# Kernel optimization log

Measured on AMD Instinct MI355X. Metric: run time of the kernel, lower is better.

Reference implementation:

```python
import jax, jax.numpy as jnp
import numpy as np
import math

H = 16          # num_attention_heads
D = 64          # attention_head_size
MAX_POS = 1024  # max_position_embeddings


def setup_inputs() -> dict:
    key = jax.random.key(0)
    ks = jax.random.split(key, 6)
    B, S, HID = 4, 1024, 1024
    scale = 1.0 / math.sqrt(HID)
    return {
        "hidden_states": jax.random.normal(ks[0], (B, S, HID), jnp.float32),
        "attention_mask": jnp.zeros((B, 1, 1, S), jnp.float32),
        "Wq": jax.random.normal(ks[1], (HID, HID), jnp.float32) * scale,
        "bq": jnp.zeros((HID,), jnp.float32),
        "Wk": jax.random.normal(ks[2], (HID, HID), jnp.float32) * scale,
        "bk": jnp.zeros((HID,), jnp.float32),
        "Wv": jax.random.normal(ks[3], (HID, HID), jnp.float32) * scale,
        "bv": jnp.zeros((HID,), jnp.float32),
        "dist_emb": jax.random.normal(ks[4], (2 * MAX_POS - 1, D), jnp.float32) * 0.02,
    }


def _split_heads(x):
    # [B,S,H*D] -> [B,H,S,D]
    B, S, _ = x.shape
    return x.reshape(B, S, H, D).transpose(0, 2, 1, 3)


def reference(hidden_states, attention_mask, Wq, bq, Wk, bk, Wv, bv, dist_emb):
    B, S, _ = hidden_states.shape
    q = _split_heads(hidden_states @ Wq.T + bq)   # [B,H,S,D]
    k = _split_heads(hidden_states @ Wk.T + bk)
    v = _split_heads(hidden_states @ Wv.T + bv)

    scores = jnp.einsum("bhqd,bhkd->bhqk", q, k)  # [B,H,S,S]

    # relative_key_query positional bias
    pos_l = jnp.arange(S)[:, None]
    pos_r = jnp.arange(S)[None, :]
    distance = pos_l - pos_r + (MAX_POS - 1)      # [S,S] in [0, 2*MAX_POS-2]
    pos_emb = dist_emb[distance]                  # [S,S,D]
    rel_q = jnp.einsum("bhld,lrd->bhlr", q, pos_emb)
    rel_k = jnp.einsum("bhrd,lrd->bhlr", k, pos_emb)
    scores = (scores + rel_q + rel_k) / math.sqrt(D)

    scores = scores + attention_mask
    probs = jax.nn.softmax(scores, axis=-1)
    ctx = jnp.einsum("bhqk,bhkd->bhqd", probs, v)  # [B,H,S,D]
    ctx = ctx.transpose(0, 2, 1, 3).reshape(B, S, H * D)
    return ctx
```

## Files before the change

### kernel.cpp

```cpp
#include <hip/hip_runtime.h>
#include <hip/hip_bf16.h>

#define B_   4
#define S_   1024
#define HID_ 1024
#define H_   16
#define D_   64

typedef __attribute__((ext_vector_type(4))) float f32x4;
typedef __attribute__((ext_vector_type(8))) __bf16 bf16v8;
typedef __attribute__((ext_vector_type(8))) unsigned short u16x8;
typedef __attribute__((ext_vector_type(4))) unsigned short u16x4;

#define MFMA16(a, b, c) __builtin_amdgcn_mfma_f32_16x16x32_bf16((a), (b), (c), 0, 0, 0)
#define GLOAD16(gp, lp)                                                              \
    __builtin_amdgcn_global_load_lds((const __attribute__((address_space(1))) void*)(gp), \
                                     (__attribute__((address_space(3))) void*)(lp), 16, 0, 0)

__device__ __forceinline__ unsigned short f2bs_hw(float f) {
    __bf16 h = (__bf16)f;
    return __builtin_bit_cast(unsigned short, h);
}
__device__ __forceinline__ unsigned pack2bf(float a, float b) {
    unsigned short lo = f2bs_hw(a), hi = f2bs_hw(b);
    return (unsigned)lo | ((unsigned)hi << 16);
}
__device__ __forceinline__ float bs2f(unsigned short s) {
    union { unsigned u; float f; } v; v.u = ((unsigned)s) << 16;
    return v.f;
}

__global__ void conv_kernel(const float* __restrict__ src, unsigned short* __restrict__ dst,
                            int n4) {
    int i = blockIdx.x * 256 + threadIdx.x;
    if (i < n4) {
        float4 x = *(const float4*)(src + (size_t)i * 4);
        uint2 o;
        o.x = pack2bf(x.x, x.y);
        o.y = pack2bf(x.z, x.w);
        *(uint2*)(dst + (size_t)i * 4) = o;
    }
}

__global__ void conv4_kernel(const float* __restrict__ Wq, const float* __restrict__ Wk,
                             const float* __restrict__ Wv, const float* __restrict__ E,
                             unsigned short* __restrict__ Wqb, unsigned short* __restrict__ Wkb,
                             unsigned short* __restrict__ Wvb, unsigned short* __restrict__ Eb) {
    int bid = blockIdx.x;
    const float* src;
    unsigned short* dst;
    int n4, base;
    if (bid < 1024)      { src = Wq; dst = Wqb; n4 = 262144; base = bid; }
    else if (bid < 2048) { src = Wk; dst = Wkb; n4 = 262144; base = bid - 1024; }
    else if (bid < 3072) { src = Wv; dst = Wvb; n4 = 262144; base = bid - 2048; }
    else                 { src = E;  dst = Eb;  n4 = 32752;  base = bid - 3072; }
    int i = base * 256 + threadIdx.x;
    if (i < n4) {
        float4 x = *(const float4*)(src + (size_t)i * 4);
        uint2 o;
        o.x = pack2bf(x.x, x.y);
        o.y = pack2bf(x.z, x.w);
        *(uint2*)(dst + (size_t)i * 4) = o;
    }
}

__global__ __launch_bounds__(256)
void proj_kernel(const unsigned short* __restrict__ Xb,
                 const unsigned short* __restrict__ Wqb, const float* __restrict__ bq,
                 const unsigned short* __restrict__ Wkb, const float* __restrict__ bk,
                 const unsigned short* __restrict__ Wvb, const float* __restrict__ bv,
                 unsigned short* __restrict__ Qo, unsigned short* __restrict__ Ko,
                 unsigned short* __restrict__ Vo)
{
    __shared__ __align__(16) unsigned short Al[2][128][64];
    __shared__ __align__(16) unsigned short Bl[2][128][64];

    const int bid = blockIdx.x;
    const int tile = (bid & 7) * 96 + (bid >> 3);
    const int rt = tile / 24, ct = tile % 24;
    const int row0 = rt * 128, col0 = ct * 128;
    const int which = col0 >> 10;
    const unsigned short* Wm = (which == 0) ? Wqb : (which == 1) ? Wkb : Wvb;
    const float* bias        = (which == 0) ? bq  : (which == 1) ? bk  : bv;
    unsigned short* Out      = (which == 0) ? Qo  : (which == 1) ? Ko  : Vo;
    const int oc0 = col0 & 1023;

    const int t = threadIdx.x;
    const int lane = t & 63, w = t >> 6;
    const int wr = w >> 1, wc = w & 1;
    const int lg = lane >> 4, lc = lane & 15;

    f32x4 acc[4][4] = {};

#pragma unroll
    for (int l = 0; l < 4; ++l) {
        int idx = l * 256 + t;
        int r = idx >> 3, su = idx & 7;
        int u = su ^ (r & 7);
        GLOAD16(Xb + (size_t)(row0 + r) * 1024 + u * 8,
                &Al[0][0][0] + (size_t)(l * 256 + w * 64) * 8);
        GLOAD16(Wm + (size_t)(oc0 + r) * 1024 + u * 8,
                &Bl[0][0][0] + (size_t)(l * 256 + w * 64) * 8);
    }

    for (int it = 0; it < 16; ++it) {
        const int p = it & 1;
        __syncthreads();
        if (it < 15) {
            const int k1 = (it + 1) * 64;
#pragma unroll
            for (int l = 0; l < 4; ++l) {
                int idx = l * 256 + t;
                int r = idx >> 3, su = idx & 7;
                int u = su ^ (r & 7);
                GLOAD16(Xb + (size_t)(row0 + r) * 1024 + k1 + u * 8,
                        &Al[p ^ 1][0][0] + (size_t)(l * 256 + w * 64) * 8);
                GLOAD16(Wm + (size_t)(oc0 + r) * 1024 + k1 + u * 8,
                        &Bl[p ^ 1][0][0] + (size_t)(l * 256 + w * 64) * 8);
            }
        }
        bf16v8 af[4][2], bfg[4][2];
#pragma unroll
        for (int m = 0; m < 4; ++m)
#pragma unroll
            for (int ks = 0; ks < 2; ++ks) {
                int u = (ks * 4 + lg) ^ (lc & 7);
                af[m][ks] = *(const bf16v8*)&Al[p][wr * 64 + m * 16 + lc][u * 8];
            }
#pragma unroll
        for (int n = 0; n < 4; ++n)
#pragma unroll
            for (int ks = 0; ks < 2; ++ks) {
                int u = (ks * 4 + lg) ^ (lc & 7);
                bfg[n][ks] = *(const bf16v8*)&Bl[p][wc * 64 + n * 16 + lc][u * 8];
            }
        __builtin_amdgcn_s_setprio(1);
#pragma unroll
        for (int m = 0; m < 4; ++m)
#pragma unroll
            for (int n = 0; n < 4; ++n) {
                acc[m][n] = MFMA16(af[m][0], bfg[n][0], acc[m][n]);
                acc[m][n] = MFMA16(af[m][1], bfg[n][1], acc[m][n]);
            }
        __builtin_amdgcn_s_setprio(0);
    }

#pragma unroll
    for (int m = 0; m < 4; ++m)
#pragma unroll
        for (int n = 0; n < 4; ++n) {
            int j = oc0 + wc * 64 + n * 16 + lc;
            int hh = j >> 6, dd = j & 63;
            float bv_ = bias[j];
#pragma unroll
            for (int r = 0; r < 4; ++r) {
                int i = row0 + wr * 64 + m * 16 + lg * 4 + r;
                int bb = i >> 10, ss = i & 1023;
                float v = acc[m][n][r] + bv_;
                Out[((size_t)(bb * 16 + hh) * 1024 + ss) * 64 + dd] = f2bs_hw(v);
            }
        }
}

__global__ __launch_bounds__(256)
void attn_kernel(const unsigned short* __restrict__ Q,
                 const unsigned short* __restrict__ K,
                 const unsigned short* __restrict__ V,
                 const float* __restrict__ mask,
                 const unsigned short* __restrict__ Eb,
                 float* __restrict__ Out)
{
    __shared__ __align__(16) unsigned short Kl[64][64];
    __shared__ __align__(16) unsigned short El[128][64];
    __shared__ __align__(16) unsigned short VTl[64][72];
    __shared__ __align__(16) unsigned short QDl[4][16][136];
    __shared__ __align__(16) unsigned short KDl[64][132];
    __shared__ __align__(16) unsigned Pex[4 * 16 * 36];
    __shared__ float maskl[64];

    const int t = threadIdx.x;
    const int lane = t & 63, w = t >> 6;
    const int lg = lane >> 4, lc = lane & 15;

    const int bid = blockIdx.x;
    const int bh = bid & 63;
    const int qt = bid >> 6;
    const int b = bh >> 4, h = bh & 15;
    const int i0 = qt * 64;
    const int i_loc = w * 16 + lc;

    const float C2 = 0.125f * 1.44269504089f;
    const float L2E = 1.44269504089f;

    const unsigned short* Qh = Q + (size_t)bh * S_ * D_;
    const unsigned short* Kh = K + (size_t)bh * S_ * D_;
    const unsigned short* Vh = V + (size_t)bh * S_ * D_;

    bf16v8 qf[2];
#pragma unroll
    for (int ks = 0; ks < 2; ++ks)
        qf[ks] = *(const bf16v8*)(Qh + (size_t)(i0 + i_loc) * D_ + ks * 32 + lg * 8);

    u16x8 ones_u;
#pragma unroll
    for (int e = 0; e < 8; ++e) ones_u[e] = 0x3F80;
    const bf16v8 onesf = __builtin_bit_cast(bf16v8, ones_u);

    float m_r = -1e30f;
    f32x4 lacc = (f32x4){0.f, 0.f, 0.f, 0.f};
    f32x4 ctx[4];
#pragma unroll
    for (int nd = 0; nd < 4; ++nd) ctx[nd] = (f32x4){0.f, 0.f, 0.f, 0.f};

    unsigned* PexW = &Pex[(w * 16 + lc) * 36];

    for (int jt = 0; jt < 16; ++jt) {
        const int j0 = jt * 64;
        const int dbase = i0 - j0 + 960;
        __syncthreads();

#pragma unroll
        for (int l = 0; l < 2; ++l) {
            int idx = l * 256 + t;
            int r = idx >> 3, su = idx & 7;
            int u = su ^ (r & 7);
            GLOAD16(Kh + (size_t)(j0 + r) * 64 + u * 8,
                    &Kl[0][0] + (size_t)(l * 256 + w * 64) * 8);
        }
        {
            int a = t & 7, rb = (t >> 3) << 1;
            int cq = a * 8;
            u16x8 v0 = *(const u16x8*)(Vh + (size_t)(j0 + rb) * 64 + cq);
            u16x8 v1 = *(const u16x8*)(Vh + (size_t)(j0 + rb + 1) * 64 + cq);
            int jst = (rb + (a << 3)) & 63;
#pragma unroll
            for (int e = 0; e < 8; ++e)
                *(unsigned*)&VTl[cq + e][jst] = (unsigned)v0[e] | ((unsigned)v1[e] << 16);
        }
        if (jt == 0) {
            const int sb0 = dbase & 127;
#pragma unroll
            for (int l = 0; l < 4; ++l) {
                int idx = l * 256 + t;
                int sl = idx >> 3, su = idx & 7;
                int u = su ^ (sl & 7);
                int dr = dbase + ((sl - sb0) & 127);
                if (dr > 2046) dr = 2046;
                GLOAD16(Eb + (size_t)dr * 64 + u * 8,
                        &El[0][0] + (size_t)(l * 256 + w * 64) * 8);
            }
        } else {
            const int sb = dbase & 127;
#pragma unroll
            for (int l = 0; l < 2; ++l) {
                int idx = l * 256 + t;
                int rl = idx >> 3, su = idx & 7;
                int u = su ^ (rl & 7);
                GLOAD16(Eb + (size_t)(dbase + rl) * 64 + u * 8,
                        &El[sb][0] + (size_t)(l * 256 + w * 64) * 8);
            }
        }
        if (t < 64) maskl[t] = mask[(size_t)b * S_ + j0 + t] * L2E;
        __syncthreads();

        bf16v8 kfa[2];
#pragma unroll
        for (int ks = 0; ks < 2; ++ks) {
            int u = (ks * 4 + lg) ^ (lc & 7);
            kfa[ks] = *(const bf16v8*)&Kl[w * 16 + lc][u * 8];
        }
        __builtin_amdgcn_s_setprio(1);
#pragma unroll
        for (int nd = 0; nd < 8; ++nd) {
            int sl = (dbase + nd * 16 + lc) & 127;
            int u0 = lg ^ (lc & 7);
            int u1 = (4 + lg) ^ (lc & 7);
            bf16v8 ef0 = *(const bf16v8*)&El[sl][u0 * 8];
            bf16v8 ef1 = *(const bf16v8*)&El[sl][u1 * 8];
            f32x4 kd = (f32x4){0.f, 0.f, 0.f, 0.f};
            kd = MFMA16(ef0, kfa[0], kd);
            kd = MFMA16(ef1, kfa[1], kd);
            uint2 pk;
            pk.x = pack2bf(kd[0], kd[1]);
            pk.y = pack2bf(kd[2], kd[3]);
            *(uint2*)&KDl[w * 16 + lc][nd * 16 + lg * 4] = pk;
            if (nd < 4 || jt == 0) {
                f32x4 qd = (f32x4){0.f, 0.f, 0.f, 0.f};
                qd = MFMA16(ef0, qf[0], qd);
                qd = MFMA16(ef1, qf[1], qd);
                int slot0 = ((dbase & 127) + nd * 16 + lg * 4) & 127;
                uint2 qk2;
                qk2.x = pack2bf(qd[0], qd[1]);
                qk2.y = pack2bf(qd[2], qd[3]);
                *(uint2*)&QDl[w][lc][slot0] = qk2;
            }
        }
        f32x4 s[4];
#pragma unroll
        for (int n = 0; n < 4; ++n) {
            s[n] = (f32x4){0.f, 0.f, 0.f, 0.f};
#pragma unroll
            for (int ks = 0; ks < 2; ++ks) {
                int u = (ks * 4 + lg) ^ (lc & 7);
                bf16v8 kb = *(const bf16v8*)&Kl[n * 16 + lc][u * 8];
                s[n] = MFMA16(kb, qf[ks], s[n]);
            }
        }
        __builtin_amdgcn_s_setprio(0);
        __syncthreads();

        const unsigned short* QDw = &QDl[w][lc][0];
        float vmax = -1e30f;
#pragma unroll
        for (int n = 0; n < 4; ++n) {
            int jb = n * 16 + lg * 4;
            float4 mk = *(const float4*)&maskl[jb];
            int kbase = jb * 131 + i_loc + 63;
            int qbase = dbase + i_loc - jb + 63;
#pragma unroll
            for (int r = 0; r < 4; ++r) {
                float qdv = bs2f(QDw[(qbase - r) & 127]);
                float kdv = bs2f((&KDl[0][0])[kbase + 131 * r]);
                float mkr = (r == 0) ? mk.x : (r == 1) ? mk.y : (r == 2) ? mk.z : mk.w;
                float val = (s[n][r] + qdv + kdv) * C2 + mkr;
                s[n][r] = val;
                vmax = fmaxf(vmax, val);
            }
        }
        vmax = fmaxf(vmax, __shfl_xor(vmax, 16));
        vmax = fmaxf(vmax, __shfl_xor(vmax, 32));

        if (__any(vmax > m_r)) {
            float mnew = fmaxf(m_r, vmax);
            float alpha = exp2f(m_r - mnew);
            m_r = mnew;
#pragma unroll
            for (int r = 0; r < 4; ++r) lacc[r] *= alpha;
#pragma unroll
            for (int nd = 0; nd < 4; ++nd)
#pragma unroll
                for (int r = 0; r < 4; ++r)
                    ctx[nd][r] *= alpha;
        }

#pragma unroll
        for (int n = 0; n < 4; ++n)
#pragma unroll
            for (int r = 0; r < 4; ++r)
                s[n][r] = exp2f(s[n][r] - m_r);

#pragma unroll
        for (int n = 0; n < 4; ++n) {
            uint2 pk;
            pk.x = pack2bf(s[n][0], s[n][1]);
            pk.y = pack2bf(s[n][2], s[n][3]);
            *(uint2*)&PexW[n * 8 + lg * 2] = pk;
        }
        bf16v8 pfB[2];
#pragma unroll
        for (int ks = 0; ks < 2; ++ks) {
            int nc = 2 * ks + (lg >> 1);
            pfB[ks] = *(const bf16v8*)&PexW[nc * 8 + (lg & 1) * 4];
        }

        __builtin_amdgcn_s_setprio(1);
        lacc = MFMA16(onesf, pfB[0], lacc);
        lacc = MFMA16(onesf, pfB[1], lacc);
#pragma unroll
        for (int nd = 0; nd < 4; ++nd) {
            int vrow = nd * 16 + lc;
#pragma unroll
            for (int ks = 0; ks < 2; ++ks) {
                int jst = (ks * 32 + lg * 8 + ((vrow >> 3) << 3)) & 63;
                bf16v8 vf = *(const bf16v8*)&VTl[vrow][jst];
                ctx[nd] = MFMA16(vf, pfB[ks], ctx[nd]);
            }
        }
        __builtin_amdgcn_s_setprio(0);
    }

    float inv = 1.0f / lacc[0];
    float* outp = Out + ((size_t)(b * S_ + i0 + i_loc) * H_ + h) * D_;
#pragma unroll
    for (int nd = 0; nd < 4; ++nd) {
        float4 o;
        o.x = ctx[nd][0] * inv;
        o.y = ctx[nd][1] * inv;
        o.z = ctx[nd][2] * inv;
        o.w = ctx[nd][3] * inv;
        *(float4*)(outp + nd * 16 + lg * 4) = o;
    }
}

extern "C" void kernel_launch(void* const* d_in, const int* in_sizes, int n_in,
                              void* d_out, int out_size, void* d_ws, size_t ws_size,
                              hipStream_t stream)
{
    const float* X    = (const float*)d_in[0];
    const float* mask = (const float*)d_in[1];
    const float* Wq   = (const float*)d_in[2];
    const float* bq   = (const float*)d_in[3];
    const float* Wk   = (const float*)d_in[4];
    const float* bk   = (const float*)d_in[5];
    const float* Wv   = (const float*)d_in[6];
    const float* bv   = (const float*)d_in[7];
    const float* E    = (const float*)d_in[8];
    float* Out = (float*)d_out;

    const size_t headN = (size_t)B_ * H_ * S_ * D_;
    unsigned short* Qw  = (unsigned short*)d_ws;
    unsigned short* Kw  = Qw + headN;
    unsigned short* Vw  = Kw + headN;
    unsigned short* Ebw = Vw + headN;
    unsigned short* Xb  = Ebw + (size_t)2047 * 64;
    unsigned short* Wqb = Xb + (size_t)4096 * 1024;
    unsigned short* Wkb = Wqb + (size_t)1024 * 1024;
    unsigned short* Wvb = Wkb + (size_t)1024 * 1024;

    conv_kernel<<<dim3(4096), dim3(256), 0, stream>>>(X, Xb, 4096 * 1024 / 4);
    conv4_kernel<<<dim3(3200), dim3(256), 0, stream>>>(Wq, Wk, Wv, E, Wqb, Wkb, Wvb, Ebw);
    proj_kernel<<<dim3(768), dim3(256), 0, stream>>>(Xb, Wqb, bq, Wkb, bk, Wvb, bv, Qw, Kw, Vw);
    attn_kernel<<<dim3(1024), dim3(256), 0, stream>>>(Qw, Kw, Vw, mask, Ebw, Out);
}
```

Before: 153.8 us.

## Merge conversion kernels and trim relative-key MFMAs to needed diagonals

Folds the X conversion into the weight/embedding conversion kernel so there is one fewer launch. In the attention kernel, each wave now computes only the 5 of 8 relative-key tiles its rows actually read, instead of all 8. The query-distance buffer gets a wrapped duplicate slot so reads need no modulo, which removes per-element masking. This saves MFMA work and index arithmetic. The cost is more intricate indexing that could go wrong at the edge diagonals.

```diff
diff --git a/kernel.cpp b/kernel.cpp
--- a/kernel.cpp
+++ b/kernel.cpp
@@ -30,30 +30,21 @@
     return v.f;
 }
 
-__global__ void conv_kernel(const float* __restrict__ src, unsigned short* __restrict__ dst,
-                            int n4) {
-    int i = blockIdx.x * 256 + threadIdx.x;
-    if (i < n4) {
-        float4 x = *(const float4*)(src + (size_t)i * 4);
-        uint2 o;
-        o.x = pack2bf(x.x, x.y);
-        o.y = pack2bf(x.z, x.w);
-        *(uint2*)(dst + (size_t)i * 4) = o;
-    }
-}
-
-__global__ void conv4_kernel(const float* __restrict__ Wq, const float* __restrict__ Wk,
-                             const float* __restrict__ Wv, const float* __restrict__ E,
-                             unsigned short* __restrict__ Wqb, unsigned short* __restrict__ Wkb,
-                             unsigned short* __restrict__ Wvb, unsigned short* __restrict__ Eb) {
+__global__ void convall_kernel(const float* __restrict__ X,
+                               const float* __restrict__ Wq, const float* __restrict__ Wk,
+                               const float* __restrict__ Wv, const float* __restrict__ E,
+                               unsigned short* __restrict__ Xb,
+                               unsigned short* __restrict__ Wqb, unsigned short* __restrict__ Wkb,
+                               unsigned short* __restrict__ Wvb, unsigned short* __restrict__ Eb) {
     int bid = blockIdx.x;
     const float* src;
     unsigned short* dst;
     int n4, base;
-    if (bid < 1024)      { src = Wq; dst = Wqb; n4 = 262144; base = bid; }
-    else if (bid < 2048) { src = Wk; dst = Wkb; n4 = 262144; base = bid - 1024; }
-    else if (bid < 3072) { src = Wv; dst = Wvb; n4 = 262144; base = bid - 2048; }
-    else                 { src = E;  dst = Eb;  n4 = 32752;  base = bid - 3072; }
+    if (bid < 4096)      { src = X;  dst = Xb;  n4 = 1048576; base = bid; }
+    else if (bid < 5120) { src = Wq; dst = Wqb; n4 = 262144;  base = bid - 4096; }
+    else if (bid < 6144) { src = Wk; dst = Wkb; n4 = 262144;  base = bid - 5120; }
+    else if (bid < 7168) { src = Wv; dst = Wvb; n4 = 262144;  base = bid - 6144; }
+    else                 { src = E;  dst = Eb;  n4 = 32752;   base = bid - 7168; }
     int i = base * 256 + threadIdx.x;
     if (i < n4) {
         float4 x = *(const float4*)(src + (size_t)i * 4);
@@ -173,7 +164,7 @@
     __shared__ __align__(16) unsigned short Kl[64][64];
     __shared__ __align__(16) unsigned short El[128][64];
     __shared__ __align__(16) unsigned short VTl[64][72];
-    __shared__ __align__(16) unsigned short QDl[4][16][136];
+    __shared__ __align__(16) unsigned short QDl[4][16][132];
     __shared__ __align__(16) unsigned short KDl[64][132];
     __shared__ __align__(16) unsigned Pex[4 * 16 * 36];
     __shared__ float maskl[64];
@@ -213,6 +204,8 @@
     for (int nd = 0; nd < 4; ++nd) ctx[nd] = (f32x4){0.f, 0.f, 0.f, 0.f};
 
     unsigned* PexW = &Pex[(w * 16 + lc) * 36];
+    unsigned short* QDrow = &QDl[w][lc][0];
+    const int keyE = lc & 7;
 
     for (int jt = 0; jt < 16; ++jt) {
         const int j0 = jt * 64;
@@ -266,25 +259,45 @@
         bf16v8 kfa[2];
 #pragma unroll
         for (int ks = 0; ks < 2; ++ks) {
-            int u = (ks * 4 + lg) ^ (lc & 7);
+            int u = (ks * 4 + lg) ^ keyE;
             kfa[ks] = *(const bf16v8*)&Kl[w * 16 + lc][u * 8];
         }
         __builtin_amdgcn_s_setprio(1);
 #pragma unroll
-        for (int nd = 0; nd < 8; ++nd) {
-            int sl = (dbase + nd * 16 + lc) & 127;
-            int u0 = lg ^ (lc & 7);
-            int u1 = (4 + lg) ^ (lc & 7);
-            bf16v8 ef0 = *(const bf16v8*)&El[sl][u0 * 8];
-            bf16v8 ef1 = *(const bf16v8*)&El[sl][u1 * 8];
+        for (int k = 0; k < 5; ++k) {
+            int ndc16 = 48 - w * 16 + k * 16;
+            int sl = (dbase + ndc16 + lc) & 127;
+            bf16v8 ef0 = *(const bf16v8*)&El[sl][(lg ^ keyE) * 8];
+            bf16v8 ef1 = *(const bf16v8*)&El[sl][((4 + lg) ^ keyE) * 8];
             f32x4 kd = (f32x4){0.f, 0.f, 0.f, 0.f};
             kd = MFMA16(ef0, kfa[0], kd);
             kd = MFMA16(ef1, kfa[1], kd);
             uint2 pk;
             pk.x = pack2bf(kd[0], kd[1]);
             pk.y = pack2bf(kd[2], kd[3]);
-            *(uint2*)&KDl[w * 16 + lc][nd * 16 + lg * 4] = pk;
-            if (nd < 4 || jt == 0) {
+            *(uint2*)&KDl[w * 16 + lc][ndc16 + lg * 4] = pk;
+        }
+#pragma unroll
+        for (int nd = 0; nd < 4; ++nd) {
+            int sl = (dbase + nd * 16 + lc) & 127;
+            bf16v8 ef0 = *(const bf16v8*)&El[sl][(lg ^ keyE) * 8];
+            bf16v8 ef1 = *(const bf16v8*)&El[sl][((4 + lg) ^ keyE) * 8];
+            f32x4 qd = (f32x4){0.f, 0.f, 0.f, 0.f};
+            qd = MFMA16(ef0, qf[0], qd);
+            qd = MFMA16(ef1, qf[1], qd);
+            int slot0 = ((dbase & 127) + nd * 16 + lg * 4) & 127;
+            uint2 qk2;
+            qk2.x = pack2bf(qd[0], qd[1]);
+            qk2.y = pack2bf(qd[2], qd[3]);
+            *(uint2*)&QDrow[slot0] = qk2;
+            if (slot0 == 0) *(uint2*)&QDrow[128] = qk2;
+        }
+        if (jt == 0) {
+#pragma unroll
+            for (int nd = 4; nd < 8; ++nd) {
+                int sl = (dbase + nd * 16 + lc) & 127;
+                bf16v8 ef0 = *(const bf16v8*)&El[sl][(lg ^ keyE) * 8];
+                bf16v8 ef1 = *(const bf16v8*)&El[sl][((4 + lg) ^ keyE) * 8];
                 f32x4 qd = (f32x4){0.f, 0.f, 0.f, 0.f};
                 qd = MFMA16(ef0, qf[0], qd);
                 qd = MFMA16(ef1, qf[1], qd);
@@ -292,7 +305,8 @@
                 uint2 qk2;
                 qk2.x = pack2bf(qd[0], qd[1]);
                 qk2.y = pack2bf(qd[2], qd[3]);
-                *(uint2*)&QDl[w][lc][slot0] = qk2;
+                *(uint2*)&QDrow[slot0] = qk2;
+                if (slot0 == 0) *(uint2*)&QDrow[128] = qk2;
             }
         }
         f32x4 s[4];
@@ -301,7 +315,7 @@
             s[n] = (f32x4){0.f, 0.f, 0.f, 0.f};
 #pragma unroll
             for (int ks = 0; ks < 2; ++ks) {
-                int u = (ks * 4 + lg) ^ (lc & 7);
+                int u = (ks * 4 + lg) ^ keyE;
                 bf16v8 kb = *(const bf16v8*)&Kl[n * 16 + lc][u * 8];
                 s[n] = MFMA16(kb, qf[ks], s[n]);
             }
@@ -309,17 +323,16 @@
         __builtin_amdgcn_s_setprio(0);
         __syncthreads();
 
-        const unsigned short* QDw = &QDl[w][lc][0];
         float vmax = -1e30f;
 #pragma unroll
         for (int n = 0; n < 4; ++n) {
             int jb = n * 16 + lg * 4;
             float4 mk = *(const float4*)&maskl[jb];
             int kbase = jb * 131 + i_loc + 63;
-            int qbase = dbase + i_loc - jb + 63;
+            int slot3 = (dbase + i_loc - jb + 60) & 127;
 #pragma unroll
             for (int r = 0; r < 4; ++r) {
-                float qdv = bs2f(QDw[(qbase - r) & 127]);
+                float qdv = bs2f(QDrow[slot3 + 3 - r]);
                 float kdv = bs2f((&KDl[0][0])[kbase + 131 * r]);
                 float mkr = (r == 0) ? mk.x : (r == 1) ? mk.y : (r == 2) ? mk.z : mk.w;
                 float val = (s[n][r] + qdv + kdv) * C2 + mkr;
@@ -417,8 +430,8 @@
     unsigned short* Wkb = Wqb + (size_t)1024 * 1024;
     unsigned short* Wvb = Wkb + (size_t)1024 * 1024;
 
-    conv_kernel<<<dim3(4096), dim3(256), 0, stream>>>(X, Xb, 4096 * 1024 / 4);
-    conv4_kernel<<<dim3(3200), dim3(256), 0, stream>>>(Wq, Wk, Wv, E, Wqb, Wkb, Wvb, Ebw);
+    convall_kernel<<<dim3(7296), dim3(256), 0, stream>>>(X, Wq, Wk, Wv, E,
+                                                         Xb, Wqb, Wkb, Wvb, Ebw);
     proj_kernel<<<dim3(768), dim3(256), 0, stream>>>(Xb, Wqb, bq, Wkb, bk, Wvb, bv, Qw, Kw, Vw);
     attn_kernel<<<dim3(1024), dim3(256), 0, stream>>>(Qw, Kw, Vw, mask, Ebw, Out);
 }
```

Result: slower. 165.9 us (+7.8%).
